# Kernel optimization log

Measured on AMD Instinct MI355X. Metric: run time of the kernel, lower is better.

## Reference

```python
import jax, jax.numpy as jnp
import numpy as np


def setup_inputs() -> dict:
    key = jax.random.key(0)
    k1, k2 = jax.random.split(key)
    N = 33554432
    x = jax.random.normal(k1, (N,), dtype=jnp.float32)
    y = jax.random.randint(k2, (N,), 0, 2, dtype=jnp.int32)
    return {"x": x, "y": y}


def reference(x, y):
    # normalize x to [0, 1]
    xmin = jnp.min(x)
    xmax = jnp.max(x) - xmin
    xn = ((x - xmin) / xmax).reshape(-1)
    # grouped means by binary label
    m0 = (y == 0)
    n0 = jnp.sum(m0).astype(xn.dtype)
    n1 = xn.shape[0] - n0
    s0 = jnp.sum(jnp.where(m0, xn, 0.0))
    s1 = jnp.sum(xn) - s0
    lbas = s0 / n0
    lhaut = s1 / n1
    # swap so lbas <= lhaut, then difference (always <= 0)
    l = jnp.minimum(lbas, lhaut) - jnp.maximum(lbas, lhaut)
    return l.reshape(1)
```

## Files before the change

kernel.cpp:

```cpp
#include <hip/hip_runtime.h>
#include <math.h>

#define NBLOCKS 4096
#define BS 256
#define K 8
#define P2BS 1024

typedef float __attribute__((ext_vector_type(4))) vfloat4;
typedef int   __attribute__((ext_vector_type(4))) vint4;

__device__ __forceinline__ void ld_nt_f4(const vfloat4* p, vfloat4& d) {
    asm volatile("global_load_dwordx4 %0, %1, off nt" : "=v"(d) : "v"(p));
}
__device__ __forceinline__ void ld_nt_i4(const vint4* p, vint4& d) {
    asm volatile("global_load_dwordx4 %0, %1, off nt" : "=v"(d) : "v"(p));
}


__global__ __launch_bounds__(BS) void risk_pass1(const float* __restrict__ x,
                                                 const int* __restrict__ y,
                                                 double* __restrict__ ws) {
    const vfloat4* __restrict__ x4 = (const vfloat4*)x;
    const vint4*   __restrict__ y4 = (const vint4*)y;

    const int base = blockIdx.x * (BS * K) + threadIdx.x;

    vfloat4 v0, v1, v2, v3, v4, v5, v6, v7;
    vint4   w0, w1, w2, w3, w4, w5, w6, w7;

    ld_nt_f4(&x4[base + 0 * BS], v0);
    ld_nt_f4(&x4[base + 1 * BS], v1);
    ld_nt_f4(&x4[base + 2 * BS], v2);
    ld_nt_f4(&x4[base + 3 * BS], v3);
    ld_nt_f4(&x4[base + 4 * BS], v4);
    ld_nt_f4(&x4[base + 5 * BS], v5);
    ld_nt_f4(&x4[base + 6 * BS], v6);
    ld_nt_f4(&x4[base + 7 * BS], v7);
    ld_nt_i4(&y4[base + 0 * BS], w0);
    ld_nt_i4(&y4[base + 1 * BS], w1);
    ld_nt_i4(&y4[base + 2 * BS], w2);
    ld_nt_i4(&y4[base + 3 * BS], w3);
    ld_nt_i4(&y4[base + 4 * BS], w4);
    ld_nt_i4(&y4[base + 5 * BS], w5);
    ld_nt_i4(&y4[base + 6 * BS], w6);
    ld_nt_i4(&y4[base + 7 * BS], w7);

    asm volatile("s_waitcnt vmcnt(0)"
                 : "+v"(v0), "+v"(v1), "+v"(v2), "+v"(v3),
                   "+v"(v4), "+v"(v5), "+v"(v6), "+v"(v7),
                   "+v"(w0), "+v"(w1), "+v"(w2), "+v"(w3),
                   "+v"(w4), "+v"(w5), "+v"(w6), "+v"(w7));

    float fs[K], ft[K], fmn[K], fmx[K];
    int   fc[K];
    {
        const vfloat4 vv[K] = {v0, v1, v2, v3, v4, v5, v6, v7};
        const vint4   wwv[K] = {w0, w1, w2, w3, w4, w5, w6, w7};
        #pragma unroll
        for (int q = 0; q < K; ++q) {
            vfloat4 v = vv[q];
            vint4   w = wwv[q];
            fs[q] = (v.x + v.y) + (v.z + v.w);
            float a  = (w.x == 0) ? v.x : 0.0f;
            float b  = (w.y == 0) ? v.y : 0.0f;
            float cc = (w.z == 0) ? v.z : 0.0f;
            float d  = (w.w == 0) ? v.w : 0.0f;
            ft[q] = (a + b) + (cc + d);
            fc[q] = (w.x == 0) + (w.y == 0) + (w.z == 0) + (w.w == 0);
            fmn[q] = fminf(fminf(v.x, v.y), fminf(v.z, v.w));
            fmx[q] = fmaxf(fmaxf(v.x, v.y), fmaxf(v.z, v.w));
        }
    }

    float s01 = fs[0] + fs[1], s23 = fs[2] + fs[3], s45 = fs[4] + fs[5], s67 = fs[6] + fs[7];
    float t01 = ft[0] + ft[1], t23 = ft[2] + ft[3], t45 = ft[4] + ft[5], t67 = ft[6] + ft[7];
    double sum  = ((double)(s01 + s23)) + ((double)(s45 + s67));
    double sum0 = ((double)(t01 + t23)) + ((double)(t45 + t67));
    int    cnt0 = ((fc[0] + fc[1]) + (fc[2] + fc[3])) + ((fc[4] + fc[5]) + (fc[6] + fc[7]));
    float  mn = fminf(fminf(fminf(fmn[0], fmn[1]), fminf(fmn[2], fmn[3])),
                      fminf(fminf(fmn[4], fmn[5]), fminf(fmn[6], fmn[7])));
    float  mx = fmaxf(fmaxf(fmaxf(fmx[0], fmx[1]), fmaxf(fmx[2], fmx[3])),
                      fmaxf(fmaxf(fmx[4], fmx[5]), fmaxf(fmx[6], fmx[7])));

    for (int off = 32; off > 0; off >>= 1) {
        sum  += __shfl_down(sum,  off);
        sum0 += __shfl_down(sum0, off);
        cnt0 += __shfl_down(cnt0, off);
        mn = fminf(mn, __shfl_down(mn, off));
        mx = fmaxf(mx, __shfl_down(mx, off));
    }

    __shared__ double s_sum[BS / 64], s_sum0[BS / 64];
    __shared__ int    s_cnt[BS / 64];
    __shared__ float  s_mn[BS / 64], s_mx[BS / 64];

    int lane = threadIdx.x & 63;
    int wave = threadIdx.x >> 6;
    if (lane == 0) {
        s_sum[wave] = sum; s_sum0[wave] = sum0; s_cnt[wave] = cnt0;
        s_mn[wave] = mn; s_mx[wave] = mx;
    }
    __syncthreads();

    if (threadIdx.x == 0) {
        double bsum = s_sum[0], bsum0 = s_sum0[0];
        int bcnt = s_cnt[0];
        float bmn = s_mn[0], bmx = s_mx[0];
        #pragma unroll
        for (int w = 1; w < BS / 64; ++w) {
            bsum += s_sum[w]; bsum0 += s_sum0[w]; bcnt += s_cnt[w];
            bmn = fminf(bmn, s_mn[w]); bmx = fmaxf(bmx, s_mx[w]);
        }
        ws[0 * NBLOCKS + blockIdx.x] = bsum;
        ws[1 * NBLOCKS + blockIdx.x] = bsum0;
        ws[2 * NBLOCKS + blockIdx.x] = (double)bcnt;
        ws[3 * NBLOCKS + blockIdx.x] = (double)bmn;
        ws[4 * NBLOCKS + blockIdx.x] = (double)bmx;
    }
}

__global__ __launch_bounds__(P2BS) void risk_pass2(const double* __restrict__ ws,
                                                   float* __restrict__ out,
                                                   long long n_total) {
    double sum = 0.0, sum0 = 0.0, cnt0 = 0.0;
    double mn =  INFINITY;
    double mx = -INFINITY;

    for (int i = threadIdx.x; i < NBLOCKS; i += P2BS) {
        sum  += ws[0 * NBLOCKS + i];
        sum0 += ws[1 * NBLOCKS + i];
        cnt0 += ws[2 * NBLOCKS + i];
        mn = fmin(mn, ws[3 * NBLOCKS + i]);
        mx = fmax(mx, ws[4 * NBLOCKS + i]);
    }

    for (int off = 32; off > 0; off >>= 1) {
        sum  += __shfl_down(sum,  off);
        sum0 += __shfl_down(sum0, off);
        cnt0 += __shfl_down(cnt0, off);
        mn = fmin(mn, __shfl_down(mn, off));
        mx = fmax(mx, __shfl_down(mx, off));
    }

    __shared__ double s_sum[P2BS / 64], s_sum0[P2BS / 64], s_cnt[P2BS / 64];
    __shared__ double s_mn[P2BS / 64], s_mx[P2BS / 64];
    int lane = threadIdx.x & 63;
    int wave = threadIdx.x >> 6;
    if (lane == 0) {
        s_sum[wave] = sum; s_sum0[wave] = sum0; s_cnt[wave] = cnt0;
        s_mn[wave] = mn; s_mx[wave] = mx;
    }
    __syncthreads();

    if (threadIdx.x == 0) {
        double tsum = s_sum[0], tsum0 = s_sum0[0], tcnt0 = s_cnt[0];
        double tmn = s_mn[0], tmx = s_mx[0];
        #pragma unroll
        for (int w = 1; w < P2BS / 64; ++w) {
            tsum += s_sum[w]; tsum0 += s_sum0[w]; tcnt0 += s_cnt[w];
            tmn = fmin(tmn, s_mn[w]); tmx = fmax(tmx, s_mx[w]);
        }
        double range = tmx - tmn;
        double n1 = (double)n_total - tcnt0;
        double sum1 = tsum - tsum0;
        double m0 = (tsum0 / tcnt0 - tmn) / range;
        double m1 = (sum1  / n1    - tmn) / range;
        double l = fmin(m0, m1) - fmax(m0, m1);
        out[0] = (float)l;
    }
}

extern "C" void kernel_launch(void* const* d_in, const int* in_sizes, int n_in,
                              void* d_out, int out_size, void* d_ws, size_t ws_size,
                              hipStream_t stream) {
    const float* x = (const float*)d_in[0];
    const int*   y = (const int*)d_in[1];
    float* out = (float*)d_out;
    double* ws = (double*)d_ws;
    long long n = (long long)in_sizes[0];

    risk_pass1<<<NBLOCKS, BS, 0, stream>>>(x, y, ws);
    risk_pass2<<<1, P2BS, 0, stream>>>(ws, out, n);
}
```

Measured before the change: 255.3 us.

## Double-buffer loads across four batches per block with half the blocks

```diff
diff --git a/kernel.cpp b/kernel.cpp
--- a/kernel.cpp
+++ b/kernel.cpp
@@ -1,10 +1,11 @@
 #include <hip/hip_runtime.h>
 #include <math.h>
 
-#define NBLOCKS 4096
+#define NB1 2048
 #define BS 256
-#define K 8
-#define P2BS 1024
+#define LQ 4
+#define NBATCH 4
+#define P2BS 512
 
 typedef float __attribute__((ext_vector_type(4))) vfloat4;
 typedef int   __attribute__((ext_vector_type(4))) vint4;
@@ -14,6 +15,61 @@
 }
 __device__ __forceinline__ void ld_nt_i4(const vint4* p, vint4& d) {
     asm volatile("global_load_dwordx4 %0, %1, off nt" : "=v"(d) : "v"(p));
+}
+
+#define ISSUE(R0, R1, R2, R3, W0, W1, W2, W3, t)                    \
+    do {                                                            \
+        const vfloat4* _px = x4 + base0 + (t) * (LQ * BS);          \
+        const vint4*   _py = y4 + base0 + (t) * (LQ * BS);          \
+        ld_nt_f4(_px + 0 * BS, R0);                                 \
+        ld_nt_f4(_px + 1 * BS, R1);                                 \
+        ld_nt_f4(_px + 2 * BS, R2);                                 \
+        ld_nt_f4(_px + 3 * BS, R3);                                 \
+        ld_nt_i4(_py + 0 * BS, W0);                                 \
+        ld_nt_i4(_py + 1 * BS, W1);                                 \
+        ld_nt_i4(_py + 2 * BS, W2);                                 \
+        ld_nt_i4(_py + 3 * BS, W3);                                 \
+    } while (0)
+
+#define WAIT_PREV(R0, R1, R2, R3, W0, W1, W2, W3)                   \
+    asm volatile("s_waitcnt vmcnt(8)"                               \
+                 : "+v"(R0), "+v"(R1), "+v"(R2), "+v"(R3),          \
+                   "+v"(W0), "+v"(W1), "+v"(W2), "+v"(W3))
+
+#define WAIT_LAST(R0, R1, R2, R3, W0, W1, W2, W3)                   \
+    asm volatile("s_waitcnt vmcnt(0)"                               \
+                 : "+v"(R0), "+v"(R1), "+v"(R2), "+v"(R3),          \
+                   "+v"(W0), "+v"(W1), "+v"(W2), "+v"(W3))
+
+__device__ __forceinline__ void consume(vfloat4 v0, vfloat4 v1, vfloat4 v2, vfloat4 v3,
+                                        vint4 w0, vint4 w1, vint4 w2, vint4 w3,
+                                        double& sum, double& sum0, int& cnt0,
+                                        float& mn, float& mx) {
+    float fs[LQ], ft[LQ], fmn[LQ], fmx[LQ];
+    int   fc[LQ];
+    const vfloat4 vv[LQ] = {v0, v1, v2, v3};
+    const vint4   ww[LQ] = {w0, w1, w2, w3};
+    #pragma unroll
+    for (int q = 0; q < LQ; ++q) {
+        vfloat4 v = vv[q];
+        vint4   w = ww[q];
+        fs[q] = (v.x + v.y) + (v.z + v.w);
+        float a  = (w.x == 0) ? v.x : 0.0f;
+        float b  = (w.y == 0) ? v.y : 0.0f;
+        float cc = (w.z == 0) ? v.z : 0.0f;
+        float d  = (w.w == 0) ? v.w : 0.0f;
+        ft[q] = (a + b) + (cc + d);
+        fc[q] = (w.x == 0) + (w.y == 0) + (w.z == 0) + (w.w == 0);
+        fmn[q] = fminf(fminf(v.x, v.y), fminf(v.z, v.w));
+        fmx[q] = fmaxf(fmaxf(v.x, v.y), fmaxf(v.z, v.w));
+    }
+    float sA = (fs[0] + fs[1]) + (fs[2] + fs[3]);
+    float tA = (ft[0] + ft[1]) + (ft[2] + ft[3]);
+    sum  += (double)sA;
+    sum0 += (double)tA;
+    cnt0 += (fc[0] + fc[1]) + (fc[2] + fc[3]);
+    mn = fminf(mn, fminf(fminf(fmn[0], fmn[1]), fminf(fmn[2], fmn[3])));
+    mx = fmaxf(mx, fmaxf(fmaxf(fmx[0], fmx[1]), fmaxf(fmx[2], fmx[3])));
 }
 
 
@@ -23,64 +79,31 @@
     const vfloat4* __restrict__ x4 = (const vfloat4*)x;
     const vint4*   __restrict__ y4 = (const vint4*)y;
 
-    const int base = blockIdx.x * (BS * K) + threadIdx.x;
-
-    vfloat4 v0, v1, v2, v3, v4, v5, v6, v7;
-    vint4   w0, w1, w2, w3, w4, w5, w6, w7;
-
-    ld_nt_f4(&x4[base + 0 * BS], v0);
-    ld_nt_f4(&x4[base + 1 * BS], v1);
-    ld_nt_f4(&x4[base + 2 * BS], v2);
-    ld_nt_f4(&x4[base + 3 * BS], v3);
-    ld_nt_f4(&x4[base + 4 * BS], v4);
-    ld_nt_f4(&x4[base + 5 * BS], v5);
-    ld_nt_f4(&x4[base + 6 * BS], v6);
-    ld_nt_f4(&x4[base + 7 * BS], v7);
-    ld_nt_i4(&y4[base + 0 * BS], w0);
-    ld_nt_i4(&y4[base + 1 * BS], w1);
-    ld_nt_i4(&y4[base + 2 * BS], w2);
-    ld_nt_i4(&y4[base + 3 * BS], w3);
-    ld_nt_i4(&y4[base + 4 * BS], w4);
-    ld_nt_i4(&y4[base + 5 * BS], w5);
-    ld_nt_i4(&y4[base + 6 * BS], w6);
-    ld_nt_i4(&y4[base + 7 * BS], w7);
-
-    asm volatile("s_waitcnt vmcnt(0)"
-                 : "+v"(v0), "+v"(v1), "+v"(v2), "+v"(v3),
-                   "+v"(v4), "+v"(v5), "+v"(v6), "+v"(v7),
-                   "+v"(w0), "+v"(w1), "+v"(w2), "+v"(w3),
-                   "+v"(w4), "+v"(w5), "+v"(w6), "+v"(w7));
-
-    float fs[K], ft[K], fmn[K], fmx[K];
-    int   fc[K];
-    {
-        const vfloat4 vv[K] = {v0, v1, v2, v3, v4, v5, v6, v7};
-        const vint4   wwv[K] = {w0, w1, w2, w3, w4, w5, w6, w7};
-        #pragma unroll
-        for (int q = 0; q < K; ++q) {
-            vfloat4 v = vv[q];
-            vint4   w = wwv[q];
-            fs[q] = (v.x + v.y) + (v.z + v.w);
-            float a  = (w.x == 0) ? v.x : 0.0f;
-            float b  = (w.y == 0) ? v.y : 0.0f;
-            float cc = (w.z == 0) ? v.z : 0.0f;
-            float d  = (w.w == 0) ? v.w : 0.0f;
-            ft[q] = (a + b) + (cc + d);
-            fc[q] = (w.x == 0) + (w.y == 0) + (w.z == 0) + (w.w == 0);
-            fmn[q] = fminf(fminf(v.x, v.y), fminf(v.z, v.w));
-            fmx[q] = fmaxf(fmaxf(v.x, v.y), fmaxf(v.z, v.w));
-        }
-    }
-
-    float s01 = fs[0] + fs[1], s23 = fs[2] + fs[3], s45 = fs[4] + fs[5], s67 = fs[6] + fs[7];
-    float t01 = ft[0] + ft[1], t23 = ft[2] + ft[3], t45 = ft[4] + ft[5], t67 = ft[6] + ft[7];
-    double sum  = ((double)(s01 + s23)) + ((double)(s45 + s67));
-    double sum0 = ((double)(t01 + t23)) + ((double)(t45 + t67));
-    int    cnt0 = ((fc[0] + fc[1]) + (fc[2] + fc[3])) + ((fc[4] + fc[5]) + (fc[6] + fc[7]));
-    float  mn = fminf(fminf(fminf(fmn[0], fmn[1]), fminf(fmn[2], fmn[3])),
-                      fminf(fminf(fmn[4], fmn[5]), fminf(fmn[6], fmn[7])));
-    float  mx = fmaxf(fmaxf(fmaxf(fmx[0], fmx[1]), fmaxf(fmx[2], fmx[3])),
-                      fmaxf(fmaxf(fmx[4], fmx[5]), fmaxf(fmx[6], fmx[7])));
+    const int base0 = blockIdx.x * (NBATCH * LQ * BS) + threadIdx.x;
+
+    vfloat4 a0, a1, a2, a3;  vint4 b0, b1, b2, b3;
+    vfloat4 c0, c1, c2, c3;  vint4 d0, d1, d2, d3;
+
+    double sum = 0.0, sum0 = 0.0;
+    int    cnt0 = 0;
+    float  mn =  INFINITY, mx = -INFINITY;
+
+    ISSUE(a0, a1, a2, a3, b0, b1, b2, b3, 0);
+
+    ISSUE(c0, c1, c2, c3, d0, d1, d2, d3, 1);
+    WAIT_PREV(a0, a1, a2, a3, b0, b1, b2, b3);
+    consume(a0, a1, a2, a3, b0, b1, b2, b3, sum, sum0, cnt0, mn, mx);
+
+    ISSUE(a0, a1, a2, a3, b0, b1, b2, b3, 2);
+    WAIT_PREV(c0, c1, c2, c3, d0, d1, d2, d3);
+    consume(c0, c1, c2, c3, d0, d1, d2, d3, sum, sum0, cnt0, mn, mx);
+
+    ISSUE(c0, c1, c2, c3, d0, d1, d2, d3, 3);
+    WAIT_PREV(a0, a1, a2, a3, b0, b1, b2, b3);
+    consume(a0, a1, a2, a3, b0, b1, b2, b3, sum, sum0, cnt0, mn, mx);
+
+    WAIT_LAST(c0, c1, c2, c3, d0, d1, d2, d3);
+    consume(c0, c1, c2, c3, d0, d1, d2, d3, sum, sum0, cnt0, mn, mx);
 
     for (int off = 32; off > 0; off >>= 1) {
         sum  += __shfl_down(sum,  off);
@@ -111,11 +134,11 @@
             bsum += s_sum[w]; bsum0 += s_sum0[w]; bcnt += s_cnt[w];
             bmn = fminf(bmn, s_mn[w]); bmx = fmaxf(bmx, s_mx[w]);
         }
-        ws[0 * NBLOCKS + blockIdx.x] = bsum;
-        ws[1 * NBLOCKS + blockIdx.x] = bsum0;
-        ws[2 * NBLOCKS + blockIdx.x] = (double)bcnt;
-        ws[3 * NBLOCKS + blockIdx.x] = (double)bmn;
-        ws[4 * NBLOCKS + blockIdx.x] = (double)bmx;
+        ws[0 * NB1 + blockIdx.x] = bsum;
+        ws[1 * NB1 + blockIdx.x] = bsum0;
+        ws[2 * NB1 + blockIdx.x] = (double)bcnt;
+        ws[3 * NB1 + blockIdx.x] = (double)bmn;
+        ws[4 * NB1 + blockIdx.x] = (double)bmx;
     }
 }
 
@@ -126,12 +149,12 @@
     double mn =  INFINITY;
     double mx = -INFINITY;
 
-    for (int i = threadIdx.x; i < NBLOCKS; i += P2BS) {
-        sum  += ws[0 * NBLOCKS + i];
-        sum0 += ws[1 * NBLOCKS + i];
-        cnt0 += ws[2 * NBLOCKS + i];
-        mn = fmin(mn, ws[3 * NBLOCKS + i]);
-        mx = fmax(mx, ws[4 * NBLOCKS + i]);
+    for (int i = threadIdx.x; i < NB1; i += P2BS) {
+        sum  += ws[0 * NB1 + i];
+        sum0 += ws[1 * NB1 + i];
+        cnt0 += ws[2 * NB1 + i];
+        mn = fmin(mn, ws[3 * NB1 + i]);
+        mx = fmax(mx, ws[4 * NB1 + i]);
     }
 
     for (int off = 32; off > 0; off >>= 1) {
@@ -179,6 +202,6 @@
     double* ws = (double*)d_ws;
     long long n = (long long)in_sizes[0];
 
-    risk_pass1<<<NBLOCKS, BS, 0, stream>>>(x, y, ws);
+    risk_pass1<<<NB1, BS, 0, stream>>>(x, y, ws);
     risk_pass2<<<1, P2BS, 0, stream>>>(ws, out, n);
 }
```

Result: no change. 251.5 us (median of 2 runs) (-1.5%).
